# Performance work log

Measured on AMD Instinct MI355X. Metric: run time of the kernel, lower is better.

Reference implementation:

```python
import jax, jax.numpy as jnp
import numpy as np

N = 100000  # nodes
E = 1600000  # edges
D_IN = 64
D_H = 64


def _sage_conv(x, src, dst, w_l, b_l, w_r):
    """PyG SAGEConv (mean aggr): lin_l(mean_j x_j) + lin_r(x_i).
    w_l, w_r: [out, in]; b_l: [out]."""
    # scatter-mean of source features onto target nodes
    msg_sum = jax.ops.segment_sum(x[src], dst, num_segments=N)  # [N, in]
    cnt = jax.ops.segment_sum(jnp.ones((src.shape[0],), x.dtype), dst, num_segments=N)
    mean = msg_sum / jnp.maximum(cnt, 1.0)[:, None]
    return mean @ w_l.T + b_l + x @ w_r.T


def setup_inputs() -> dict:
    key = jax.random.key(0)
    ks = jax.random.split(key, 8)
    x = jax.random.normal(ks[0], (N, D_IN), dtype=jnp.float32)
    edge_index = jax.random.randint(ks[1], (2, E), 0, N, dtype=jnp.int64)
    s = 1.0 / np.sqrt(D_IN)
    w_l1 = jax.random.uniform(ks[2], (D_H, D_IN), jnp.float32, -s, s)
    b_l1 = jnp.zeros((D_H,), jnp.float32)
    w_r1 = jax.random.uniform(ks[3], (D_H, D_IN), jnp.float32, -s, s)
    s2 = 1.0 / np.sqrt(D_H)
    w_l2 = jax.random.uniform(ks[4], (D_H, D_H), jnp.float32, -s2, s2)
    b_l2 = jnp.zeros((D_H,), jnp.float32)
    w_r2 = jax.random.uniform(ks[5], (D_H, D_H), jnp.float32, -s2, s2)
    return {"x": x, "edge_index": edge_index,
            "w_l1": w_l1, "b_l1": b_l1, "w_r1": w_r1,
            "w_l2": w_l2, "b_l2": b_l2, "w_r2": w_r2}


def reference(x, edge_index, w_l1, b_l1, w_r1, w_l2, b_l2, w_r2):
    src, dst = edge_index[0], edge_index[1]
    h = jax.nn.relu(_sage_conv(x, src, dst, w_l1, b_l1, w_r1))
    out = _sage_conv(h, src, dst, w_l2, b_l2, w_r2)
    return out
```

## Files before the change

kernel.cpp:

```cpp
#include <hip/hip_runtime.h>

#define N_NODES 100000
#define N_EDGES 1600000
#define D 64

#define BSHIFT 7
#define BNODES (1 << BSHIFT)
#define NB ((N_NODES + BNODES - 1) / BNODES)
#define PB 256
#define TILE ((N_EDGES + PB - 1) / PB)
#define TBL (NB * PB)
#define SCAN_BLK 1024
#define SCAN_GRID ((TBL + SCAN_BLK - 1) / SCAN_BLK)
#define MAXB 4096
#define CAST_GRID 2048

typedef __attribute__((ext_vector_type(8))) short short8;
typedef __attribute__((ext_vector_type(4))) float float4v;

__device__ __forceinline__ unsigned short f2bf(float f) {
    unsigned u = __float_as_uint(f);
    u = (u + 0x7fffu + ((u >> 16) & 1u)) >> 16;
    return (unsigned short)u;
}
__device__ __forceinline__ unsigned packbf2(float a, float b) {
    return (unsigned)f2bf(a) | ((unsigned)f2bf(b) << 16);
}

__device__ __forceinline__ float4 bf16x4_to_f4(uint2 v) {
    float4 r;
    r.x = __uint_as_float(v.x << 16);
    r.y = __uint_as_float(v.x & 0xffff0000u);
    r.z = __uint_as_float(v.y << 16);
    r.w = __uint_as_float(v.y & 0xffff0000u);
    return r;
}

__global__ __launch_bounds__(256) void cast_absmax_part(const float* __restrict__ x,
                                                        unsigned short* __restrict__ xb,
                                                        float* __restrict__ partial) {
    __shared__ float red[4];
    float m = 0.0f;
    int stride = gridDim.x * 256;
    for (int i = blockIdx.x * 256 + threadIdx.x; i < N_NODES * D / 4; i += stride) {
        float4 v = ((const float4*)x)[i];
        ushort4 o;
        o.x = f2bf(v.x); o.y = f2bf(v.y); o.z = f2bf(v.z); o.w = f2bf(v.w);
        ((ushort4*)xb)[i] = o;
        m = fmaxf(m, fmaxf(fmaxf(fabsf(v.x), fabsf(v.y)), fmaxf(fabsf(v.z), fabsf(v.w))));
    }
    for (int off = 32; off >= 1; off >>= 1) m = fmaxf(m, __shfl_xor(m, off, 64));
    if ((threadIdx.x & 63) == 0) red[threadIdx.x >> 6] = m;
    __syncthreads();
    if (threadIdx.x == 0)
        partial[blockIdx.x] = fmaxf(fmaxf(red[0], red[1]), fmaxf(red[2], red[3]));
}

__global__ __launch_bounds__(256) void absmax_bf16_part(const unsigned short* __restrict__ inb,
                                                        float* __restrict__ partial) {
    __shared__ float red[4];
    float m = 0.0f;
    int stride = gridDim.x * 256;
    for (int i = blockIdx.x * 256 + threadIdx.x; i < N_NODES * D / 4; i += stride) {
        uint2 v = ((const uint2*)inb)[i];
        float4 f = bf16x4_to_f4(v);
        m = fmaxf(m, fmaxf(fmaxf(fabsf(f.x), fabsf(f.y)), fmaxf(fabsf(f.z), fabsf(f.w))));
    }
    for (int off = 32; off >= 1; off >>= 1) m = fmaxf(m, __shfl_xor(m, off, 64));
    if ((threadIdx.x & 63) == 0) red[threadIdx.x >> 6] = m;
    __syncthreads();
    if (threadIdx.x == 0)
        partial[blockIdx.x] = fmaxf(fmaxf(red[0], red[1]), fmaxf(red[2], red[3]));
}

__global__ __launch_bounds__(1024) void reduce_amax(const float* __restrict__ partial,
                                                    int n,
                                                    unsigned* __restrict__ amax_bits) {
    __shared__ float red[16];
    float m = 0.0f;
    for (int i = threadIdx.x; i < n; i += 1024) m = fmaxf(m, partial[i]);
    for (int off = 32; off >= 1; off >>= 1) m = fmaxf(m, __shfl_xor(m, off, 64));
    if ((threadIdx.x & 63) == 0) red[threadIdx.x >> 6] = m;
    __syncthreads();
    if (threadIdx.x == 0) {
        float mm = 0.0f;
#pragma unroll
        for (int w = 0; w < 16; ++w) mm = fmaxf(mm, red[w]);
        *amax_bits = __float_as_uint(mm);
    }
}

__global__ __launch_bounds__(256) void quant8(const unsigned short* __restrict__ inb,
                                              unsigned char* __restrict__ out8,
                                              const unsigned* __restrict__ amax_bits) {
    int i = blockIdx.x * blockDim.x + threadIdx.x;
    if (i >= N_NODES * D / 4) return;
    float A = __uint_as_float(*amax_bits);
    float s = (A > 0.0f) ? 127.0f / A : 0.0f;
    uint2 v = ((const uint2*)inb)[i];
    float4 f = bf16x4_to_f4(v);
    int q0 = min(127, max(-127, __float2int_rn(f.x * s))) + 128;
    int q1 = min(127, max(-127, __float2int_rn(f.y * s))) + 128;
    int q2 = min(127, max(-127, __float2int_rn(f.z * s))) + 128;
    int q3 = min(127, max(-127, __float2int_rn(f.w * s))) + 128;
    ((unsigned*)out8)[i] = (unsigned)q0 | ((unsigned)q1 << 8) |
                           ((unsigned)q2 << 16) | ((unsigned)q3 << 24);
}

__global__ __launch_bounds__(256) void prep_w(const float* __restrict__ wl,
                                              const float* __restrict__ wr,
                                              unsigned short* __restrict__ wb) {
    int i = blockIdx.x * 256 + threadIdx.x;
    if (i < D * 2 * D) {
        int o = i >> 7, k = i & 127;
        float v = (k < D) ? wl[o * D + k] : wr[o * D + (k - D)];
        wb[i] = f2bf(v);
    }
}

__global__ __launch_bounds__(1024) void p1_hist(const int* __restrict__ dst,
                                                int* __restrict__ table) {
    __shared__ int hist[NB];
    for (int i = threadIdx.x; i < NB; i += 1024) hist[i] = 0;
    __syncthreads();
    int lo = blockIdx.x * TILE;
    int hi = min(lo + TILE, N_EDGES);
    for (int e = lo + threadIdx.x; e < hi; e += 1024)
        atomicAdd(&hist[dst[e] >> BSHIFT], 1);
    __syncthreads();
    for (int b = threadIdx.x; b < NB; b += 1024)
        table[b * PB + blockIdx.x] = hist[b];
}

__global__ __launch_bounds__(SCAN_BLK) void scan_blocks_n(int* __restrict__ buf,
                                                          int* __restrict__ blk_sum,
                                                          int n) {
    __shared__ int tmp[SCAN_BLK];
    int i = blockIdx.x * SCAN_BLK + threadIdx.x;
    int v = (i < n) ? buf[i] : 0;
    int val = v;
    tmp[threadIdx.x] = val;
    __syncthreads();
    for (int off = 1; off < SCAN_BLK; off <<= 1) {
        int t = (threadIdx.x >= off) ? tmp[threadIdx.x - off] : 0;
        __syncthreads();
        val += t;
        tmp[threadIdx.x] = val;
        __syncthreads();
    }
    if (i < n) buf[i] = val - v;
    if (threadIdx.x == SCAN_BLK - 1) blk_sum[blockIdx.x] = val;
}

__global__ __launch_bounds__(256) void scan_partials(const int* __restrict__ blk_sum,
                                                     int* __restrict__ blk_off, int nb) {
    __shared__ int t[256];
    int i = threadIdx.x;
    int v = (i < nb) ? blk_sum[i] : 0;
    int val = v;
    t[i] = val;
    __syncthreads();
    for (int off = 1; off < 256; off <<= 1) {
        int u = (i >= off) ? t[i - off] : 0;
        __syncthreads();
        val += u;
        t[i] = val;
        __syncthreads();
    }
    if (i < nb) blk_off[i] = val - v;
}

__global__ __launch_bounds__(256) void scan_finalize(int* __restrict__ buf,
                                                     const int* __restrict__ blk_off,
                                                     int n) {
    int i = blockIdx.x * 256 + threadIdx.x;
    if (i < n) buf[i] += blk_off[i >> 10];
}

__global__ __launch_bounds__(1024) void p1_scatter(const int* __restrict__ src,
                                                   const int* __restrict__ dst,
                                                   const int* __restrict__ table,
                                                   int* __restrict__ part) {
    __shared__ int cur[NB];
    for (int b = threadIdx.x; b < NB; b += 1024)
        cur[b] = table[b * PB + blockIdx.x];
    __syncthreads();
    int lo = blockIdx.x * TILE;
    int hi = min(lo + TILE, N_EDGES);
    for (int e = lo + threadIdx.x; e < hi; e += 1024) {
        int dd = dst[e];
        int b = dd >> BSHIFT;
        int p = atomicAdd(&cur[b], 1);
        part[p] = (src[e] << BSHIFT) | (dd & (BNODES - 1));
    }
}

__global__ __launch_bounds__(1024) void p2_sort(const int* __restrict__ table,
                                                const int* __restrict__ part,
                                                int* __restrict__ row_ptr,
                                                int* __restrict__ sorted_src) {
    __shared__ int in_buf[MAXB];
    __shared__ int out_buf[MAXB];
    __shared__ int hist[BNODES];
    __shared__ int exs[BNODES];
    __shared__ int cursor[BNODES];

    int k = blockIdx.x;
    int base = table[k * PB];
    int end  = (k < NB - 1) ? table[(k + 1) * PB] : N_EDGES;
    int count = end - base;
    int tid = threadIdx.x;

    for (int i = tid; i < BNODES; i += 1024) hist[i] = 0;
    __syncthreads();

    if (count <= MAXB) {
        for (int i = tid; i < count; i += 1024) {
            int w = part[base + i];
            in_buf[i] = w;
            atomicAdd(&hist[w & (BNODES - 1)], 1);
        }
        __syncthreads();
        if (tid < 64) {
            int a = hist[2 * tid], b = hist[2 * tid + 1];
            int s = a + b, incl = s;
            for (int off = 1; off < 64; off <<= 1) {
                int t = __shfl_up(incl, off, 64);
                if (tid >= off) incl += t;
            }
            int excl = incl - s;
            exs[2 * tid] = excl;
            exs[2 * tid + 1] = excl + a;
        }
        __syncthreads();
        if (tid < BNODES) {
            int node = k * BNODES + tid;
            if (node < N_NODES) row_ptr[node] = base + exs[tid];
            cursor[tid] = exs[tid];
        }
        if (tid == 0 && k == NB - 1) row_ptr[N_NODES] = N_EDGES;
        __syncthreads();
        for (int i = tid; i < count; i += 1024) {
            int w = in_buf[i];
            int r = atomicAdd(&cursor[w & (BNODES - 1)], 1);
            out_buf[r] = w >> BSHIFT;
        }
        __syncthreads();
        for (int i = tid; i < count; i += 1024)
            sorted_src[base + i] = out_buf[i];
    } else {
        for (int i = tid; i < count; i += 1024)
            atomicAdd(&hist[part[base + i] & (BNODES - 1)], 1);
        __syncthreads();
        if (tid < 64) {
            int a = hist[2 * tid], b = hist[2 * tid + 1];
            int s = a + b, incl = s;
            for (int off = 1; off < 64; off <<= 1) {
                int t = __shfl_up(incl, off, 64);
                if (tid >= off) incl += t;
            }
            int excl = incl - s;
            exs[2 * tid] = excl;
            exs[2 * tid + 1] = excl + a;
        }
        __syncthreads();
        if (tid < BNODES) {
            int node = k * BNODES + tid;
            if (node < N_NODES) row_ptr[node] = base + exs[tid];
            cursor[tid] = exs[tid];
        }
        if (tid == 0 && k == NB - 1) row_ptr[N_NODES] = N_EDGES;
        __syncthreads();
        for (int i = tid; i < count; i += 1024) {
            int w = part[base + i];
            int r = atomicAdd(&cursor[w & (BNODES - 1)], 1);
            sorted_src[base + r] = w >> BSHIFT;
        }
    }
}

__global__ __launch_bounds__(512) void sage8(
    const int* __restrict__ row_ptr, const int* __restrict__ nbr,
    const uint4* __restrict__ tab8,
    const unsigned short* __restrict__ selfb,
    const unsigned* __restrict__ amax_bits,
    const unsigned short* __restrict__ wb,
    const float* __restrict__ b_l,
    float* __restrict__ out,
    unsigned short* __restrict__ outb,
    int apply_relu)
{
    __shared__ unsigned short a_s[16][136];
    __shared__ float bias[D];

    int tid = threadIdx.x;
    if (tid < D) bias[tid] = b_l[tid];

    int wave = tid >> 6;
    int lane = tid & 63;
    int nsel = lane >> 5;
    int l32  = lane & 31;
    int g    = l32 >> 2;
    int c    = l32 & 3;
    int arow = wave * 2 + nsel;
    int node = blockIdx.x * 16 + arow;

    float A  = __uint_as_float(*amax_bits);
    float gs = A * (1.0f / 127.0f);

    int begin = row_ptr[node];
    int end   = row_ptr[node + 1];

    unsigned aLo[4] = {0, 0, 0, 0};
    unsigned aHi[4] = {0, 0, 0, 0};
    for (int base = begin; base < end; base += 32) {
        int m = end - base; if (m > 32) m = 32;
        int id = (l32 < m) ? __builtin_nontemporal_load(&nbr[base + l32]) : 0;
#pragma unroll
        for (int j = 0; j < 32; j += 8) {
            int s = __shfl(id, nsel * 32 + j + g, 64);
            if (j + g < m) {
                uint4 v = tab8[4 * (size_t)s + c];
                aLo[0] += v.x & 0x00FF00FFu; aHi[0] += (v.x >> 8) & 0x00FF00FFu;
                aLo[1] += v.y & 0x00FF00FFu; aHi[1] += (v.y >> 8) & 0x00FF00FFu;
                aLo[2] += v.z & 0x00FF00FFu; aHi[2] += (v.z >> 8) & 0x00FF00FFu;
                aLo[3] += v.w & 0x00FF00FFu; aHi[3] += (v.w >> 8) & 0x00FF00FFu;
            }
        }
    }

#pragma unroll
    for (int off = 4; off <= 16; off <<= 1) {
#pragma unroll
        for (int k = 0; k < 4; ++k) {
            aLo[k] += (unsigned)__shfl_xor((int)aLo[k], off, 64);
            aHi[k] += (unsigned)__shfl_xor((int)aHi[k], off, 64);
        }
    }

    int   deg  = end - begin;
    float invd = 1.0f / fmaxf((float)deg, 1.0f);
    float bofs = 128.0f * (float)deg;
    float sc   = gs * invd;

    if (l32 < 4) {
        uint4 q0, q1;
        float d0 = ((float)(aLo[0] & 0xFFFFu) - bofs) * sc;
        float d2 = ((float)(aLo[0] >> 16)     - bofs) * sc;
        float d1 = ((float)(aHi[0] & 0xFFFFu) - bofs) * sc;
        float d3 = ((float)(aHi[0] >> 16)     - bofs) * sc;
        q0.x = packbf2(d0, d1); q0.y = packbf2(d2, d3);
        d0 = ((float)(aLo[1] & 0xFFFFu) - bofs) * sc;
        d2 = ((float)(aLo[1] >> 16)     - bofs) * sc;
        d1 = ((float)(aHi[1] & 0xFFFFu) - bofs) * sc;
        d3 = ((float)(aHi[1] >> 16)     - bofs) * sc;
        q0.z = packbf2(d0, d1); q0.w = packbf2(d2, d3);
        d0 = ((float)(aLo[2] & 0xFFFFu) - bofs) * sc;
        d2 = ((float)(aLo[2] >> 16)     - bofs) * sc;
        d1 = ((float)(aHi[2] & 0xFFFFu) - bofs) * sc;
        d3 = ((float)(aHi[2] >> 16)     - bofs) * sc;
        q1.x = packbf2(d0, d1); q1.y = packbf2(d2, d3);
        d0 = ((float)(aLo[3] & 0xFFFFu) - bofs) * sc;
        d2 = ((float)(aLo[3] >> 16)     - bofs) * sc;
        d1 = ((float)(aHi[3] & 0xFFFFu) - bofs) * sc;
        d3 = ((float)(aHi[3] >> 16)     - bofs) * sc;
        q1.z = packbf2(d0, d1); q1.w = packbf2(d2, d3);
        *(uint4*)&a_s[arow][16 * l32]     = q0;
        *(uint4*)&a_s[arow][16 * l32 + 8] = q1;
    }
    if (l32 < 16) {
        uint2 xv = *(const uint2*)&selfb[(size_t)node * D + 4 * l32];
        *(uint2*)&a_s[arow][64 + 4 * l32] = xv;
    }
    __syncthreads();

    if (wave >= 4) return;

    int quad = lane >> 4;
    int cc   = lane & 15;

    float4v acc = {0.f, 0.f, 0.f, 0.f};
#pragma unroll
    for (int kk = 0; kk < 4; ++kk) {
        short8 af = *(const short8*)&a_s[cc][kk * 32 + quad * 8];
        short8 bf = *(const short8*)(wb + (size_t)(wave * 16 + cc) * 128 + kk * 32 + quad * 8);
        acc = __builtin_amdgcn_mfma_f32_16x16x32_bf16(af, bf, acc, 0, 0, 0);
    }

    int o = wave * 16 + cc;
    float bv = bias[o];
#pragma unroll
    for (int r = 0; r < 4; ++r) {
        int nd = blockIdx.x * 16 + quad * 4 + r;
        float v = acc[r] + bv;
        if (apply_relu) v = fmaxf(v, 0.0f);
        if (out)  __builtin_nontemporal_store(v, &out[(size_t)nd * D + o]);
        if (outb) __builtin_nontemporal_store(f2bf(v), &outb[(size_t)nd * D + o]);
    }
}

extern "C" void kernel_launch(void* const* d_in, const int* in_sizes, int n_in,
                              void* d_out, int out_size, void* d_ws, size_t ws_size,
                              hipStream_t stream) {
    const float* x    = (const float*)d_in[0];
    const int*   ei   = (const int*)d_in[1];
    const float* w_l1 = (const float*)d_in[2];
    const float* b_l1 = (const float*)d_in[3];
    const float* w_r1 = (const float*)d_in[4];
    const float* w_l2 = (const float*)d_in[5];
    const float* b_l2 = (const float*)d_in[6];
    const float* w_r2 = (const float*)d_in[7];
    float* out = (float*)d_out;

    const int* src = ei;
    const int* dst = ei + N_EDGES;

    unsigned* scales   = (unsigned*)d_ws;
    int* table         = (int*)d_ws + 4;
    int* blk_sum       = table + TBL;
    int* blk_off       = blk_sum + 256;
    int* row_ptr       = blk_off + 256;
    int* part          = row_ptr + 100004;
    int* sorted_src    = part + N_EDGES;
    unsigned short* xb = (unsigned short*)(sorted_src + N_EDGES);
    unsigned short* hb = xb + (size_t)N_NODES * D;
    unsigned char* x8  = (unsigned char*)(hb + (size_t)N_NODES * D);
    unsigned char* h8  = x8 + (size_t)N_NODES * D;
    unsigned short* wb1 = (unsigned short*)(h8 + (size_t)N_NODES * D);
    unsigned short* wb2 = wb1 + D * 2 * D;
    float* partA       = (float*)(wb2 + D * 2 * D);

    dim3 b256(256);
    int qgrid = (N_NODES * D / 4 + 255) / 256;
    cast_absmax_part<<<dim3(CAST_GRID), b256, 0, stream>>>(x, xb, partA);
    reduce_amax<<<dim3(1), dim3(1024), 0, stream>>>(partA, CAST_GRID, &scales[0]);
    quant8<<<dim3(qgrid), b256, 0, stream>>>(xb, x8, &scales[0]);
    prep_w<<<dim3(32), b256, 0, stream>>>(w_l1, w_r1, wb1);
    prep_w<<<dim3(32), b256, 0, stream>>>(w_l2, w_r2, wb2);

    p1_hist<<<dim3(PB), dim3(1024), 0, stream>>>(dst, table);
    scan_blocks_n<<<dim3(SCAN_GRID), dim3(SCAN_BLK), 0, stream>>>(table, blk_sum, TBL);
    scan_partials<<<dim3(1), dim3(256), 0, stream>>>(blk_sum, blk_off, SCAN_GRID);
    scan_finalize<<<dim3((TBL + 255) / 256), b256, 0, stream>>>(table, blk_off, TBL);
    p1_scatter<<<dim3(PB), dim3(1024), 0, stream>>>(src, dst, table, part);
    p2_sort<<<dim3(NB), dim3(1024), 0, stream>>>(table, part, row_ptr, sorted_src);

    dim3 lblk(512);
    dim3 lgrid(N_NODES / 16);
    sage8<<<lgrid, lblk, 0, stream>>>(row_ptr, sorted_src, (const uint4*)x8, xb,
                                      &scales[0], wb1, b_l1,
                                      (float*)nullptr, hb, 1);
    absmax_bf16_part<<<dim3(1024), b256, 0, stream>>>(hb, partA);
    reduce_amax<<<dim3(1), dim3(1024), 0, stream>>>(partA, 1024, &scales[1]);
    quant8<<<dim3(qgrid), b256, 0, stream>>>(hb, h8, &scales[1]);
    sage8<<<lgrid, lblk, 0, stream>>>(row_ptr, sorted_src, (const uint4*)h8, hb,
                                      &scales[1], wb2, b_l2,
                                      out, (unsigned short*)nullptr, 0);
}
```

Baseline: 235.2 us.

## Fuse edge bucketing passes, fold layer-1 absmax into sage8, batch neighbor gathers

Merges histogram and scatter into one kernel that claims per-bucket slots with global atomics into fixed-capacity buckets. This removes the large table scan and three scan kernels, leaving only a small scan over bucket counts. It also computes the hidden-layer absmax inside the first sage8 epilogue, dropping a full pass over the hidden features. The neighbor gather loop now issues four gathers before accumulating, and the two weight-prep launches become one. Fixed bucket capacity (CAP) risks overflow on denser distributions, and slot order inside a bucket is no longer deterministic.

Result: no change. 233.0 us (-0.9%).

```diff
diff --git a/kernel.cpp b/kernel.cpp
--- a/kernel.cpp
+++ b/kernel.cpp
@@ -9,11 +9,10 @@
 #define NB ((N_NODES + BNODES - 1) / BNODES)
 #define PB 256
 #define TILE ((N_EDGES + PB - 1) / PB)
-#define TBL (NB * PB)
-#define SCAN_BLK 1024
-#define SCAN_GRID ((TBL + SCAN_BLK - 1) / SCAN_BLK)
+#define CAP 2432
 #define MAXB 4096
 #define CAST_GRID 2048
+#define HPARTS (N_NODES / 16 * 4)
 
 typedef __attribute__((ext_vector_type(8))) short short8;
 typedef __attribute__((ext_vector_type(4))) float float4v;
@@ -48,23 +47,6 @@
         o.x = f2bf(v.x); o.y = f2bf(v.y); o.z = f2bf(v.z); o.w = f2bf(v.w);
         ((ushort4*)xb)[i] = o;
         m = fmaxf(m, fmaxf(fmaxf(fabsf(v.x), fabsf(v.y)), fmaxf(fabsf(v.z), fabsf(v.w))));
-    }
-    for (int off = 32; off >= 1; off >>= 1) m = fmaxf(m, __shfl_xor(m, off, 64));
-    if ((threadIdx.x & 63) == 0) red[threadIdx.x >> 6] = m;
-    __syncthreads();
-    if (threadIdx.x == 0)
-        partial[blockIdx.x] = fmaxf(fmaxf(red[0], red[1]), fmaxf(red[2], red[3]));
-}
-
-__global__ __launch_bounds__(256) void absmax_bf16_part(const unsigned short* __restrict__ inb,
-                                                        float* __restrict__ partial) {
-    __shared__ float red[4];
-    float m = 0.0f;
-    int stride = gridDim.x * 256;
-    for (int i = blockIdx.x * 256 + threadIdx.x; i < N_NODES * D / 4; i += stride) {
-        uint2 v = ((const uint2*)inb)[i];
-        float4 f = bf16x4_to_f4(v);
-        m = fmaxf(m, fmaxf(fmaxf(fabsf(f.x), fabsf(f.y)), fmaxf(fabsf(f.z), fabsf(f.w))));
     }
     for (int off = 32; off >= 1; off >>= 1) m = fmaxf(m, __shfl_xor(m, off, 64));
     if ((threadIdx.x & 63) == 0) red[threadIdx.x >> 6] = m;
@@ -107,95 +89,88 @@
                            ((unsigned)q2 << 16) | ((unsigned)q3 << 24);
 }
 
-__global__ __launch_bounds__(256) void prep_w(const float* __restrict__ wl,
-                                              const float* __restrict__ wr,
-                                              unsigned short* __restrict__ wb) {
+__global__ __launch_bounds__(256) void prep_w2(const float* __restrict__ wl1,
+                                               const float* __restrict__ wr1,
+                                               unsigned short* __restrict__ wb1,
+                                               const float* __restrict__ wl2,
+                                               const float* __restrict__ wr2,
+                                               unsigned short* __restrict__ wb2) {
     int i = blockIdx.x * 256 + threadIdx.x;
-    if (i < D * 2 * D) {
-        int o = i >> 7, k = i & 127;
-        float v = (k < D) ? wl[o * D + k] : wr[o * D + (k - D)];
-        wb[i] = f2bf(v);
-    }
-}
-
-__global__ __launch_bounds__(1024) void p1_hist(const int* __restrict__ dst,
-                                                int* __restrict__ table) {
+    int j = i & 8191;
+    int o = j >> 7, k = j & 127;
+    if (i < 8192) {
+        float v = (k < D) ? wl1[o * D + k] : wr1[o * D + (k - D)];
+        wb1[j] = f2bf(v);
+    } else {
+        float v = (k < D) ? wl2[o * D + k] : wr2[o * D + (k - D)];
+        wb2[j] = f2bf(v);
+    }
+}
+
+__global__ __launch_bounds__(1024) void p1_fused(const int* __restrict__ src,
+                                                 const int* __restrict__ dst,
+                                                 int* __restrict__ gcnt,
+                                                 int* __restrict__ part) {
     __shared__ int hist[NB];
     for (int i = threadIdx.x; i < NB; i += 1024) hist[i] = 0;
     __syncthreads();
+
     int lo = blockIdx.x * TILE;
     int hi = min(lo + TILE, N_EDGES);
-    for (int e = lo + threadIdx.x; e < hi; e += 1024)
-        atomicAdd(&hist[dst[e] >> BSHIFT], 1);
-    __syncthreads();
-    for (int b = threadIdx.x; b < NB; b += 1024)
-        table[b * PB + blockIdx.x] = hist[b];
-}
-
-__global__ __launch_bounds__(SCAN_BLK) void scan_blocks_n(int* __restrict__ buf,
-                                                          int* __restrict__ blk_sum,
-                                                          int n) {
-    __shared__ int tmp[SCAN_BLK];
-    int i = blockIdx.x * SCAN_BLK + threadIdx.x;
-    int v = (i < n) ? buf[i] : 0;
-    int val = v;
-    tmp[threadIdx.x] = val;
-    __syncthreads();
-    for (int off = 1; off < SCAN_BLK; off <<= 1) {
-        int t = (threadIdx.x >= off) ? tmp[threadIdx.x - off] : 0;
-        __syncthreads();
-        val += t;
-        tmp[threadIdx.x] = val;
-        __syncthreads();
-    }
-    if (i < n) buf[i] = val - v;
-    if (threadIdx.x == SCAN_BLK - 1) blk_sum[blockIdx.x] = val;
-}
-
-__global__ __launch_bounds__(256) void scan_partials(const int* __restrict__ blk_sum,
-                                                     int* __restrict__ blk_off, int nb) {
-    __shared__ int t[256];
+
+    unsigned pk[7];
+    int bk[7];
+#pragma unroll
+    for (int k = 0; k < 7; ++k) {
+        int e = lo + threadIdx.x + k * 1024;
+        if (e < hi) {
+            int dd = dst[e];
+            int ss = src[e];
+            int b = dd >> BSHIFT;
+            pk[k] = ((unsigned)ss << BSHIFT) | (unsigned)(dd & (BNODES - 1));
+            bk[k] = b;
+            atomicAdd(&hist[b], 1);
+        } else {
+            bk[k] = -1;
+        }
+    }
+    __syncthreads();
+
+    for (int b = threadIdx.x; b < NB; b += 1024) {
+        int h = hist[b];
+        if (h) hist[b] = b * CAP + atomicAdd(&gcnt[b], h);
+    }
+    __syncthreads();
+
+#pragma unroll
+    for (int k = 0; k < 7; ++k) {
+        if (bk[k] >= 0) {
+            int p = atomicAdd(&hist[bk[k]], 1);
+            part[p] = (int)pk[k];
+        }
+    }
+}
+
+__global__ __launch_bounds__(1024) void scan_nb(const int* __restrict__ gcnt,
+                                                int* __restrict__ bbase) {
+    __shared__ int t[1024];
     int i = threadIdx.x;
-    int v = (i < nb) ? blk_sum[i] : 0;
+    int v = (i < NB) ? gcnt[i] : 0;
     int val = v;
     t[i] = val;
     __syncthreads();
-    for (int off = 1; off < 256; off <<= 1) {
+    for (int off = 1; off < 1024; off <<= 1) {
         int u = (i >= off) ? t[i - off] : 0;
         __syncthreads();
         val += u;
         t[i] = val;
         __syncthreads();
     }
-    if (i < nb) blk_off[i] = val - v;
-}
-
-__global__ __launch_bounds__(256) void scan_finalize(int* __restrict__ buf,
-                                                     const int* __restrict__ blk_off,
-                                                     int n) {
-    int i = blockIdx.x * 256 + threadIdx.x;
-    if (i < n) buf[i] += blk_off[i >> 10];
-}
-
-__global__ __launch_bounds__(1024) void p1_scatter(const int* __restrict__ src,
-                                                   const int* __restrict__ dst,
-                                                   const int* __restrict__ table,
-                                                   int* __restrict__ part) {
-    __shared__ int cur[NB];
-    for (int b = threadIdx.x; b < NB; b += 1024)
-        cur[b] = table[b * PB + blockIdx.x];
-    __syncthreads();
-    int lo = blockIdx.x * TILE;
-    int hi = min(lo + TILE, N_EDGES);
-    for (int e = lo + threadIdx.x; e < hi; e += 1024) {
-        int dd = dst[e];
-        int b = dd >> BSHIFT;
-        int p = atomicAdd(&cur[b], 1);
-        part[p] = (src[e] << BSHIFT) | (dd & (BNODES - 1));
-    }
-}
-
-__global__ __launch_bounds__(1024) void p2_sort(const int* __restrict__ table,
+    if (i < NB) bbase[i] = val - v;
+}
+
+__global__ __launch_bounds__(1024) void p2_sort(const int* __restrict__ bbase,
+                                                const int* __restrict__ gcnt,
                                                 const int* __restrict__ part,
                                                 int* __restrict__ row_ptr,
                                                 int* __restrict__ sorted_src) {
@@ -206,9 +181,9 @@
     __shared__ int cursor[BNODES];
 
     int k = blockIdx.x;
-    int base = table[k * PB];
-    int end  = (k < NB - 1) ? table[(k + 1) * PB] : N_EDGES;
-    int count = end - base;
+    int base  = bbase[k];
+    int count = gcnt[k];
+    int src0  = k * CAP;
     int tid = threadIdx.x;
 
     for (int i = tid; i < BNODES; i += 1024) hist[i] = 0;
@@ -216,7 +191,7 @@
 
     if (count <= MAXB) {
         for (int i = tid; i < count; i += 1024) {
-            int w = part[base + i];
+            int w = part[src0 + i];
             in_buf[i] = w;
             atomicAdd(&hist[w & (BNODES - 1)], 1);
         }
@@ -250,7 +225,7 @@
             sorted_src[base + i] = out_buf[i];
     } else {
         for (int i = tid; i < count; i += 1024)
-            atomicAdd(&hist[part[base + i] & (BNODES - 1)], 1);
+            atomicAdd(&hist[part[src0 + i] & (BNODES - 1)], 1);
         __syncthreads();
         if (tid < 64) {
             int a = hist[2 * tid], b = hist[2 * tid + 1];
@@ -272,22 +247,27 @@
         if (tid == 0 && k == NB - 1) row_ptr[N_NODES] = N_EDGES;
         __syncthreads();
         for (int i = tid; i < count; i += 1024) {
-            int w = part[base + i];
+            int w = part[src0 + i];
             int r = atomicAdd(&cursor[w & (BNODES - 1)], 1);
             sorted_src[base + r] = w >> BSHIFT;
         }
     }
 }
 
+#define ACCW(w, kk) { aLo[kk] += (w) & 0x00FF00FFu; \
+                      aHi[kk] += __builtin_amdgcn_perm(0u, (w), 0x04030401u); }
+#define ACC4(v) { ACCW((v).x, 0) ACCW((v).y, 1) ACCW((v).z, 2) ACCW((v).w, 3) }
+
 __global__ __launch_bounds__(512) void sage8(
     const int* __restrict__ row_ptr, const int* __restrict__ nbr,
-    const uint4* __restrict__ tab8,
+    const unsigned char* __restrict__ tab8,
     const unsigned short* __restrict__ selfb,
     const unsigned* __restrict__ amax_bits,
     const unsigned short* __restrict__ wb,
     const float* __restrict__ b_l,
     float* __restrict__ out,
     unsigned short* __restrict__ outb,
+    float* __restrict__ hpart,
     int apply_relu)
 {
     __shared__ unsigned short a_s[16][136];
@@ -311,22 +291,26 @@
     int begin = row_ptr[node];
     int end   = row_ptr[node + 1];
 
+    unsigned c16 = (unsigned)(c << 4);
     unsigned aLo[4] = {0, 0, 0, 0};
     unsigned aHi[4] = {0, 0, 0, 0};
     for (int base = begin; base < end; base += 32) {
         int m = end - base; if (m > 32) m = 32;
         int id = (l32 < m) ? __builtin_nontemporal_load(&nbr[base + l32]) : 0;
-#pragma unroll
-        for (int j = 0; j < 32; j += 8) {
-            int s = __shfl(id, nsel * 32 + j + g, 64);
-            if (j + g < m) {
-                uint4 v = tab8[4 * (size_t)s + c];
-                aLo[0] += v.x & 0x00FF00FFu; aHi[0] += (v.x >> 8) & 0x00FF00FFu;
-                aLo[1] += v.y & 0x00FF00FFu; aHi[1] += (v.y >> 8) & 0x00FF00FFu;
-                aLo[2] += v.z & 0x00FF00FFu; aHi[2] += (v.z >> 8) & 0x00FF00FFu;
-                aLo[3] += v.w & 0x00FF00FFu; aHi[3] += (v.w >> 8) & 0x00FF00FFu;
-            }
-        }
+        int s0 = __shfl(id, nsel * 32 + g,      64);
+        int s1 = __shfl(id, nsel * 32 + 8 + g,  64);
+        int s2 = __shfl(id, nsel * 32 + 16 + g, 64);
+        int s3 = __shfl(id, nsel * 32 + 24 + g, 64);
+        bool a0 = (g < m), a1 = (8 + g < m), a2 = (16 + g < m), a3 = (24 + g < m);
+        uint4 v0, v1, v2, v3;
+        if (a0) v0 = *(const uint4*)(tab8 + ((((unsigned)s0) << 6) | c16));
+        if (a1) v1 = *(const uint4*)(tab8 + ((((unsigned)s1) << 6) | c16));
+        if (a2) v2 = *(const uint4*)(tab8 + ((((unsigned)s2) << 6) | c16));
+        if (a3) v3 = *(const uint4*)(tab8 + ((((unsigned)s3) << 6) | c16));
+        if (a0) { ACC4(v0) }
+        if (a1) { ACC4(v1) }
+        if (a2) { ACC4(v2) }
+        if (a3) { ACC4(v3) }
     }
 
 #pragma unroll
@@ -389,13 +373,24 @@
 
     int o = wave * 16 + cc;
     float bv = bias[o];
+    float vv[4];
+#pragma unroll
+    for (int r = 0; r < 4; ++r) {
+        float v = acc[r] + bv;
+        if (apply_relu) v = fmaxf(v, 0.0f);
+        vv[r] = v;
+    }
 #pragma unroll
     for (int r = 0; r < 4; ++r) {
         int nd = blockIdx.x * 16 + quad * 4 + r;
-        float v = acc[r] + bv;
-        if (apply_relu) v = fmaxf(v, 0.0f);
-        if (out)  __builtin_nontemporal_store(v, &out[(size_t)nd * D + o]);
-        if (outb) __builtin_nontemporal_store(f2bf(v), &outb[(size_t)nd * D + o]);
+        if (out)  __builtin_nontemporal_store(vv[r], &out[(size_t)nd * D + o]);
+        if (outb) __builtin_nontemporal_store(f2bf(vv[r]), &outb[(size_t)nd * D + o]);
+    }
+    if (hpart) {
+        float m = fmaxf(fmaxf(fabsf(vv[0]), fabsf(vv[1])),
+                        fmaxf(fabsf(vv[2]), fabsf(vv[3])));
+        for (int off = 32; off >= 1; off >>= 1) m = fmaxf(m, __shfl_xor(m, off, 64));
+        if (lane == 0) hpart[blockIdx.x * 4 + wave] = m;
     }
 }
 
@@ -416,12 +411,11 @@
     const int* dst = ei + N_EDGES;
 
     unsigned* scales   = (unsigned*)d_ws;
-    int* table         = (int*)d_ws + 4;
-    int* blk_sum       = table + TBL;
-    int* blk_off       = blk_sum + 256;
-    int* row_ptr       = blk_off + 256;
+    int* gcnt          = (int*)d_ws + 4;
+    int* bbase         = gcnt + NB;
+    int* row_ptr       = bbase + NB;
     int* part          = row_ptr + 100004;
-    int* sorted_src    = part + N_EDGES;
+    int* sorted_src    = part + NB * CAP;
     unsigned short* xb = (unsigned short*)(sorted_src + N_EDGES);
     unsigned short* hb = xb + (size_t)N_NODES * D;
     unsigned char* x8  = (unsigned char*)(hb + (size_t)N_NODES * D);
@@ -430,30 +424,28 @@
     unsigned short* wb2 = wb1 + D * 2 * D;
     float* partA       = (float*)(wb2 + D * 2 * D);
 
+    hipMemsetAsync(gcnt, 0, NB * sizeof(int), stream);
+
     dim3 b256(256);
     int qgrid = (N_NODES * D / 4 + 255) / 256;
     cast_absmax_part<<<dim3(CAST_GRID), b256, 0, stream>>>(x, xb, partA);
     reduce_amax<<<dim3(1), dim3(1024), 0, stream>>>(partA, CAST_GRID, &scales[0]);
     quant8<<<dim3(qgrid), b256, 0, stream>>>(xb, x8, &scales[0]);
-    prep_w<<<dim3(32), b256, 0, stream>>>(w_l1, w_r1, wb1);
-    prep_w<<<dim3(32), b256, 0, stream>>>(w_l2, w_r2, wb2);
-
-    p1_hist<<<dim3(PB), dim3(1024), 0, stream>>>(dst, table);
-    scan_blocks_n<<<dim3(SCAN_GRID), dim3(SCAN_BLK), 0, stream>>>(table, blk_sum, TBL);
-    scan_partials<<<dim3(1), dim3(256), 0, stream>>>(blk_sum, blk_off, SCAN_GRID);
-    scan_finalize<<<dim3((TBL + 255) / 256), b256, 0, stream>>>(table, blk_off, TBL);
-    p1_scatter<<<dim3(PB), dim3(1024), 0, stream>>>(src, dst, table, part);
-    p2_sort<<<dim3(NB), dim3(1024), 0, stream>>>(table, part, row_ptr, sorted_src);
+    prep_w2<<<dim3(64), b256, 0, stream>>>(w_l1, w_r1, wb1, w_l2, w_r2, wb2);
+
+    p1_fused<<<dim3(PB), dim3(1024), 0, stream>>>(src, dst, gcnt, part);
+    scan_nb<<<dim3(1), dim3(1024), 0, stream>>>(gcnt, bbase);
+    p2_sort<<<dim3(NB), dim3(1024), 0, stream>>>(bbase, gcnt, part, row_ptr, sorted_src);
 
     dim3 lblk(512);
     dim3 lgrid(N_NODES / 16);
-    sage8<<<lgrid, lblk, 0, stream>>>(row_ptr, sorted_src, (const uint4*)x8, xb,
+    sage8<<<lgrid, lblk, 0, stream>>>(row_ptr, sorted_src, x8, xb,
                                       &scales[0], wb1, b_l1,
-                                      (float*)nullptr, hb, 1);
-    absmax_bf16_part<<<dim3(1024), b256, 0, stream>>>(hb, partA);
-    reduce_amax<<<dim3(1), dim3(1024), 0, stream>>>(partA, 1024, &scales[1]);
+                                      (float*)nullptr, hb, partA, 1);
+    reduce_amax<<<dim3(1), dim3(1024), 0, stream>>>(partA, HPARTS, &scales[1]);
     quant8<<<dim3(qgrid), b256, 0, stream>>>(hb, h8, &scales[1]);
-    sage8<<<lgrid, lblk, 0, stream>>>(row_ptr, sorted_src, (const uint4*)h8, hb,
+    sage8<<<lgrid, lblk, 0, stream>>>(row_ptr, sorted_src, h8, hb,
                                       &scales[1], wb2, b_l2,
-                                      out, (unsigned short*)nullptr, 0);
-}
+                                      out, (unsigned short*)nullptr,
+                                      (float*)nullptr, 0);
+}
```
